# Optimization experiments

Hardware: AMD Instinct MI355X
Metric: run time of the kernel (lower is better)

## Reference

```python
import jax, jax.numpy as jnp
import numpy as np


def setup_inputs() -> dict:
    key = jax.random.key(0)
    k1, k2 = jax.random.split(key)
    pred = jax.random.normal(k1, (4, 4096, 3), dtype=jnp.float32)
    gt = jax.random.normal(k2, (4, 4096, 3), dtype=jnp.float32)
    return {"pred": pred, "gt": gt}


def reference(pred, gt):
    # Chamfer distance with L1 (Manhattan) point-to-point distance.
    # pred: [B, N, 3], gt: [B, M, 3]
    # d[b, n, m] = sum_c |pred[b,n,c] - gt[b,m,c]|
    d = jnp.abs(pred[:, :, None, :] - gt[:, None, :, :]).sum(-1)  # [B, N, M]
    cham_x = d.min(axis=2).mean(axis=1)  # nearest gt for each pred point, [B]
    cham_y = d.min(axis=1).mean(axis=1)  # nearest pred for each gt point, [B]
    # point_reduction='mean' per direction, batch_reduction='mean' (pytorch3d default)
    return jnp.mean(cham_x + cham_y)
```

## Files before the change

### kernel.cpp

```cpp
#include <hip/hip_runtime.h>
#include <cfloat>


constexpr int TPB = 256;
constexpr int PTS = 4;
constexpr int NC  = TPB * PTS;
constexpr int MC  = 256;

__global__ __launch_bounds__(TPB) void chamfer_partial_kernel(
    const float* __restrict__ pred, const float* __restrict__ gt,
    float* __restrict__ partial, int B, int N, int M) {
    const int dir = blockIdx.z;
    const int b   = blockIdx.y;
    const float* q = dir ? gt   : pred;
    const float* t = dir ? pred : gt;
    const int Nq   = dir ? M : N;
    const int Nt   = dir ? N : M;
    const int nchunks = Nq / NC;
    const int nc = blockIdx.x % nchunks;
    const int mc = blockIdx.x / nchunks;

    __shared__ float4 lds4[MC];

    const float* tbase = t + ((size_t)b * Nt + (size_t)mc * MC) * 3;
    for (int i = threadIdx.x; i < MC * 3; i += TPB) {
        ((float*)&lds4[i / 3])[i % 3] = tbase[i];
    }
    __syncthreads();

    const float* qb = q + (size_t)b * Nq * 3;
    float px[PTS], py[PTS], pz[PTS], mn[PTS];
    int n[PTS];
#pragma unroll
    for (int i = 0; i < PTS; ++i) {
        n[i] = nc * NC + threadIdx.x + i * TPB;
        px[i] = qb[n[i] * 3 + 0];
        py[i] = qb[n[i] * 3 + 1];
        pz[i] = qb[n[i] * 3 + 2];
        mn[i] = FLT_MAX;
    }

#pragma unroll 8
    for (int j = 0; j < MC; ++j) {
        float4 g = lds4[j];
#pragma unroll
        for (int i = 0; i < PTS; ++i) {
            float d = fabsf(px[i] - g.x) + fabsf(py[i] - g.y) + fabsf(pz[i] - g.z);
            mn[i] = fminf(mn[i], d);
        }
    }

    float* outp = partial + (((size_t)mc * 2 + dir) * B + b) * N;
#pragma unroll
    for (int i = 0; i < PTS; ++i) outp[n[i]] = mn[i];
}

__global__ __launch_bounds__(256) void chamfer_reduce_kernel(
    const float* __restrict__ partial, float* __restrict__ out,
    int Q, int nmc, float inv) {
    const int qidx = blockIdx.x * 256 + threadIdx.x;
    float mn = FLT_MAX;
#pragma unroll
    for (int mc = 0; mc < 16; ++mc)
        mn = fminf(mn, partial[(size_t)mc * Q + qidx]);
    float v = mn * inv;

    for (int off = 32; off > 0; off >>= 1) v += __shfl_down(v, off, 64);
    __shared__ float red[4];
    const int lane = threadIdx.x & 63, w = threadIdx.x >> 6;
    if (lane == 0) red[w] = v;
    __syncthreads();
    if (threadIdx.x == 0)
        atomicAdd(out, red[0] + red[1] + red[2] + red[3]);
}

extern "C" void kernel_launch(void* const* d_in, const int* in_sizes, int n_in,
                              void* d_out, int out_size, void* d_ws, size_t ws_size,
                              hipStream_t stream) {
    const float* pred = (const float*)d_in[0];
    const float* gt   = (const float*)d_in[1];
    float* out = (float*)d_out;

    const int B = 4;
    const int N = in_sizes[0] / (B * 3);
    const int M = in_sizes[1] / (B * 3);

    float* partial = (float*)d_ws;
    const int nmc = M / MC;
    const int Q = 2 * B * N;

    hipMemsetAsync(out, 0, sizeof(float), stream);

    dim3 grid((N / NC) * nmc, B, 2);
    chamfer_partial_kernel<<<grid, TPB, 0, stream>>>(pred, gt, partial, B, N, M);

    chamfer_reduce_kernel<<<Q / 256, 256, 0, stream>>>(
        partial, out, Q, nmc, 1.0f / (float)(B * N));
}
```

Measured before the change: 77.70 us.

## Read target points via uniform scalar loads instead of LDS, halve points per thread

Removes the shared-memory staging of target points and its barrier. Each thread now reads target coordinates directly from global memory with wave-uniform addresses, which the compiler can turn into scalar loads, and processes two targets per iteration. Points per thread drop from 4 to 2, doubling the grid to raise parallelism. The risk is scalar-load latency and lower arithmetic reuse per target load.

```diff
diff --git a/kernel.cpp b/kernel.cpp
--- a/kernel.cpp
+++ b/kernel.cpp
@@ -3,7 +3,7 @@
 
 
 constexpr int TPB = 256;
-constexpr int PTS = 4;
+constexpr int PTS = 2;
 constexpr int NC  = TPB * PTS;
 constexpr int MC  = 256;
 
@@ -12,23 +12,17 @@
     float* __restrict__ partial, int B, int N, int M) {
     const int dir = blockIdx.z;
     const int b   = blockIdx.y;
-    const float* q = dir ? gt   : pred;
-    const float* t = dir ? pred : gt;
+    const float* __restrict__ q = dir ? gt   : pred;
+    const float* __restrict__ t = dir ? pred : gt;
     const int Nq   = dir ? M : N;
     const int Nt   = dir ? N : M;
     const int nchunks = Nq / NC;
     const int nc = blockIdx.x % nchunks;
     const int mc = blockIdx.x / nchunks;
 
-    __shared__ float4 lds4[MC];
+    const float* __restrict__ tb = t + ((size_t)b * Nt + (size_t)mc * MC) * 3;
+    const float* __restrict__ qb = q + (size_t)b * Nq * 3;
 
-    const float* tbase = t + ((size_t)b * Nt + (size_t)mc * MC) * 3;
-    for (int i = threadIdx.x; i < MC * 3; i += TPB) {
-        ((float*)&lds4[i / 3])[i % 3] = tbase[i];
-    }
-    __syncthreads();
-
-    const float* qb = q + (size_t)b * Nq * 3;
     float px[PTS], py[PTS], pz[PTS], mn[PTS];
     int n[PTS];
 #pragma unroll
@@ -41,12 +35,14 @@
     }
 
 #pragma unroll 8
-    for (int j = 0; j < MC; ++j) {
-        float4 g = lds4[j];
+    for (int j = 0; j < MC; j += 2) {
+        const float gx0 = tb[j * 3 + 0], gy0 = tb[j * 3 + 1], gz0 = tb[j * 3 + 2];
+        const float gx1 = tb[j * 3 + 3], gy1 = tb[j * 3 + 4], gz1 = tb[j * 3 + 5];
 #pragma unroll
         for (int i = 0; i < PTS; ++i) {
-            float d = fabsf(px[i] - g.x) + fabsf(py[i] - g.y) + fabsf(pz[i] - g.z);
-            mn[i] = fminf(mn[i], d);
+            float d0 = fabsf(px[i] - gx0) + fabsf(py[i] - gy0) + fabsf(pz[i] - gz0);
+            float d1 = fabsf(px[i] - gx1) + fabsf(py[i] - gy1) + fabsf(pz[i] - gz1);
+            mn[i] = fminf(mn[i], fminf(d0, d1));
         }
     }
 
@@ -57,7 +53,7 @@
 
 __global__ __launch_bounds__(256) void chamfer_reduce_kernel(
     const float* __restrict__ partial, float* __restrict__ out,
-    int Q, int nmc, float inv) {
+    int Q, float inv) {
     const int qidx = blockIdx.x * 256 + threadIdx.x;
     float mn = FLT_MAX;
 #pragma unroll
@@ -86,14 +82,13 @@
     const int M = in_sizes[1] / (B * 3);
 
     float* partial = (float*)d_ws;
-    const int nmc = M / MC;
     const int Q = 2 * B * N;
 
     hipMemsetAsync(out, 0, sizeof(float), stream);
 
-    dim3 grid((N / NC) * nmc, B, 2);
+    dim3 grid((N / NC) * (M / MC), B, 2);
     chamfer_partial_kernel<<<grid, TPB, 0, stream>>>(pred, gt, partial, B, N, M);
 
     chamfer_reduce_kernel<<<Q / 256, 256, 0, stream>>>(
-        partial, out, Q, nmc, 1.0f / (float)(B * N));
+        partial, out, Q, 1.0f / (float)(B * N));
 }
```

Result: slower. 80.64 us (+3.8%).
